# Kernel tuning notes

Hardware: AMD Instinct MI355X
Metric: run time of the kernel (lower is better)

Reference implementation:

```python
import jax, jax.numpy as jnp
import numpy as np

N, D, H, DEG = 20000, 128, 128, 32


def setup_inputs() -> dict:
    key = jax.random.key(0)
    ks = jax.random.split(key, 6)
    s = 0.02
    h = jax.random.normal(ks[0], (N, D), dtype=jnp.float32)
    # per-node neighbor indices, sorted by index (permutation invariance per docstring)
    nbr_idx = jnp.sort(jax.random.randint(ks[1], (N, DEG), 0, N), axis=-1)
    W_ih = jax.random.normal(ks[2], (4 * H, D), dtype=jnp.float32) * s
    W_hh = jax.random.normal(ks[3], (4 * H, H), dtype=jnp.float32) * s
    b_ih = jnp.zeros((4 * H,), jnp.float32)
    b_hh = jnp.zeros((4 * H,), jnp.float32)
    W_out = jax.random.normal(ks[4], (H, D + H), dtype=jnp.float32) * s
    b_out = jnp.zeros((H,), jnp.float32)
    return {"h": h, "nbr_idx": nbr_idx, "W_ih": W_ih, "W_hh": W_hh,
            "b_ih": b_ih, "b_hh": b_hh, "W_out": W_out, "b_out": b_out}


def reference(h, nbr_idx, W_ih, W_hh, b_ih, b_hh, W_out, b_out):
    # Gather neighbor features: [N, DEG, D]
    nbr = h[nbr_idx]
    # Precompute input-to-gate projections for all steps: [N, DEG, 4H]
    xg = jnp.einsum('ndi,gi->ndg', nbr, W_ih) + b_ih + b_hh
    xg = jnp.swapaxes(xg, 0, 1)  # [DEG, N, 4H] for scan over neighbor sequence
    h0 = jnp.zeros((h.shape[0], W_hh.shape[1]), h.dtype)
    c0 = jnp.zeros_like(h0)

    def step(carry, g_t):
        hp, cp = carry
        g = g_t + hp @ W_hh.T            # [N, 4H]
        i, f, gg, o = jnp.split(g, 4, axis=-1)  # PyTorch gate order i,f,g,o
        c = jax.nn.sigmoid(f) * cp + jax.nn.sigmoid(i) * jnp.tanh(gg)
        hn = jax.nn.sigmoid(o) * jnp.tanh(c)
        return (hn, c), None

    (agg, _), _ = jax.lax.scan(step, (h0, c0), xg)  # agg = final hidden state [N, H]
    combined = jnp.concatenate([h, agg], axis=-1)   # [N, D+H]
    return jax.nn.relu(combined @ W_out.T + b_out)  # [N, H]
```

## Files before the change

### kernel.cpp

```cpp
#include <hip/hip_runtime.h>

#define NN 20000
#define DD 128
#define HH 128
#define G4 512
#define DEG 32
#define NPB 32
#define PAIRS 625
#define GRID2 512
#define XTRA (PAIRS-GRID2)

typedef __attribute__((ext_vector_type(4))) float f32x4;
typedef __attribute__((ext_vector_type(8))) short s16x8;

#ifndef __has_builtin
#define __has_builtin(x) 0
#endif

static __device__ __forceinline__ float fexp2(float x){
#if __has_builtin(__builtin_amdgcn_exp2f)
  return __builtin_amdgcn_exp2f(x);
#else
  return exp2f(x);
#endif
}
static __device__ __forceinline__ float frcp(float x){
#if __has_builtin(__builtin_amdgcn_rcpf)
  return __builtin_amdgcn_rcpf(x);
#else
  return 1.f/x;
#endif
}

static __device__ __forceinline__ unsigned cvt_pk_bf16(float lo, float hi){
  unsigned r;
  asm("v_cvt_pk_bf16_f32 %0, %1, %2" : "=v"(r) : "v"(lo), "v"(hi));
  return r;
}
static __device__ __forceinline__ s16x8 ld8bf(const float* __restrict__ p){
  f32x4 a = *(const f32x4*)p;
  f32x4 b = *(const f32x4*)(p+4);
  union{unsigned u[4]; s16x8 v;} z;
  z.u[0]=cvt_pk_bf16(a[0],a[1]);
  z.u[1]=cvt_pk_bf16(a[2],a[3]);
  z.u[2]=cvt_pk_bf16(b[0],b[1]);
  z.u[3]=cvt_pk_bf16(b[2],b[3]);
  return z.v;
}
static __device__ __forceinline__ float lo16f(unsigned u){
  union{unsigned x; float f;} v; v.x = u << 16; return v.f;
}
static __device__ __forceinline__ float hi16f(unsigned u){
  union{unsigned x; float f;} v; v.x = u & 0xffff0000u; return v.f;
}
#define NLOG2E -1.44269504f
#define TLOG2E  2.88539008f

__global__ __launch_bounds__(512,2) void k_hp(
    const float* __restrict__ h, const float* __restrict__ W_ih,
    const float* __restrict__ b_ih, const float* __restrict__ b_hh,
    unsigned short* __restrict__ Hp)
{
  const int tid=threadIdx.x, w=tid>>6, lane=tid&63, lo=lane&15, hi=lane>>4;
  s16x8 A[4][4];
#pragma unroll
  for(int g=0;g<4;++g){
    const float* wr=W_ih+(size_t)(128*g+16*w+lo)*DD+8*hi;
#pragma unroll
    for(int c=0;c<4;++c) A[g][c]=ld8bf(wr+32*c);
  }
  f32x4 bb[4];
#pragma unroll
  for(int g=0;g<4;++g){
    const int gcb=128*g+16*w+4*hi;
    bb[g]=*(const f32x4*)(b_ih+gcb) + *(const f32x4*)(b_hh+gcb);
  }
  const int nchunk = (blockIdx.x < 57) ? 2 : 1;
  for(int cc=0; cc<nchunk; ++cc){
    const int n0 = ((cc? 256+blockIdx.x : blockIdx.x))*64;
    f32x4 acc[4][4];
#pragma unroll
    for(int g=0;g<4;++g)
#pragma unroll
      for(int nt=0;nt<4;++nt) acc[g][nt]=(f32x4)0.f;
#pragma unroll
    for(int c=0;c<4;++c){
      s16x8 B[4];
#pragma unroll
      for(int nt=0;nt<4;++nt){
        int nd=n0+16*nt+lo; if(nd>=NN) nd=NN-1;
        B[nt]=ld8bf(h+(size_t)nd*DD+32*c+8*hi);
      }
#pragma unroll
      for(int g=0;g<4;++g)
#pragma unroll
        for(int nt=0;nt<4;++nt)
          acc[g][nt]=__builtin_amdgcn_mfma_f32_16x16x32_bf16(A[g][c],B[nt],acc[g][nt],0,0,0);
    }
#pragma unroll
    for(int nt=0;nt<4;++nt){
      int nd=n0+16*nt+lo;
      if(nd<NN){
        unsigned short* p = Hp + (size_t)nd*G4 + w*64 + hi*16;
        uint4 q0, q1;
        q0.x=cvt_pk_bf16(acc[0][nt][0]+bb[0][0], acc[0][nt][1]+bb[0][1]);
        q0.y=cvt_pk_bf16(acc[0][nt][2]+bb[0][2], acc[0][nt][3]+bb[0][3]);
        q0.z=cvt_pk_bf16(acc[1][nt][0]+bb[1][0], acc[1][nt][1]+bb[1][1]);
        q0.w=cvt_pk_bf16(acc[1][nt][2]+bb[1][2], acc[1][nt][3]+bb[1][3]);
        q1.x=cvt_pk_bf16(acc[2][nt][0]+bb[2][0], acc[2][nt][1]+bb[2][1]);
        q1.y=cvt_pk_bf16(acc[2][nt][2]+bb[2][2], acc[2][nt][3]+bb[2][3]);
        q1.z=cvt_pk_bf16(acc[3][nt][0]+bb[3][0], acc[3][nt][1]+bb[3][1]);
        q1.w=cvt_pk_bf16(acc[3][nt][2]+bb[3][2], acc[3][nt][3]+bb[3][3]);
        *(uint4*)p = q0;
        *(uint4*)(p+8) = q1;
      }
    }
  }
}

static __device__ __forceinline__ void unpack_acc(const uint4 q[2], f32x4 acc[4]){
  acc[0][0]=lo16f(q[0].x); acc[0][1]=hi16f(q[0].x); acc[0][2]=lo16f(q[0].y); acc[0][3]=hi16f(q[0].y);
  acc[1][0]=lo16f(q[0].z); acc[1][1]=hi16f(q[0].z); acc[1][2]=lo16f(q[0].w); acc[1][3]=hi16f(q[0].w);
  acc[2][0]=lo16f(q[1].x); acc[2][1]=hi16f(q[1].x); acc[2][2]=lo16f(q[1].y); acc[2][3]=hi16f(q[1].y);
  acc[3][0]=lo16f(q[1].z); acc[3][1]=hi16f(q[1].z); acc[3][2]=lo16f(q[1].w); acc[3][3]=hi16f(q[1].w);
}

__global__ __launch_bounds__(512,2) void k_lstm(
    const float* __restrict__ h, const int* __restrict__ nbr,
    const float* __restrict__ W_hh, const unsigned short* __restrict__ Hp,
    const float* __restrict__ W_out, const float* __restrict__ b_out,
    float* __restrict__ out)
{
  __shared__ unsigned short hpA[16*HH];
  __shared__ unsigned short hpB[16*HH];
  __shared__ int nlds[DEG*NPB];
  const int tid=threadIdx.x, w=tid>>6, lane=tid&63, lo=lane&15, hi=lane>>4;
  const int swz=(lo&7)<<4;

  s16x8 A[4][4];
#pragma unroll
  for(int g=0;g<4;++g){
    const float* wr=W_hh+(size_t)(128*g+16*w+lo)*HH+8*hi;
#pragma unroll
    for(int c=0;c<4;++c) A[g][c]=ld8bf(wr+32*c);
  }

  const int npair = (blockIdx.x < XTRA) ? 2 : 1;
  for(int pp=0; pp<npair; ++pp){
    const int pidx = pp ? (GRID2 + blockIdx.x) : blockIdx.x;
    const int n0 = pidx*NPB;

    __syncthreads();
    {
      unsigned* za=(unsigned*)&hpA[0];
      unsigned* zb=(unsigned*)&hpB[0];
      za[tid]=0u; za[tid+512]=0u;
      zb[tid]=0u; zb[tid+512]=0u;
#pragma unroll
      for(int i=0;i<2;++i){
        int idx=tid+512*i;
        nlds[(idx&31)*NPB + (idx>>5)] = nbr[n0*DEG + idx];
      }
    }
    __syncthreads();

    float cstA[4]={0.f,0.f,0.f,0.f}, cstB[4]={0.f,0.f,0.f,0.f};
    f32x4 accB[4];
#pragma unroll
    for(int g=0;g<4;++g) accB[g]=(f32x4)0.f;

    uint4 qA0[2], qA1[2], qB0[2], qB1[2];
    {
      int ia0=nlds[lo],        ib0=nlds[16+lo];
      int ia1=nlds[NPB+lo],    ib1=nlds[NPB+16+lo];
      const unsigned short* g0=Hp+(size_t)ia0*G4+w*64+hi*16;
      const unsigned short* g1=Hp+(size_t)ib0*G4+w*64+hi*16;
      const unsigned short* g2=Hp+(size_t)ia1*G4+w*64+hi*16;
      const unsigned short* g3=Hp+(size_t)ib1*G4+w*64+hi*16;
      qA0[0]=*(const uint4*)g0; qA0[1]=*(const uint4*)(g0+8);
      qB0[0]=*(const uint4*)g1; qB0[1]=*(const uint4*)(g1+8);
      qA1[0]=*(const uint4*)g2; qA1[1]=*(const uint4*)(g2+8);
      qB1[0]=*(const uint4*)g3; qB1[1]=*(const uint4*)(g3+8);
    }

    for(int t=0;t<DEG;++t){
      const int tn2 = (t+2<DEG)? t+2 : DEG-1;
      int ia2=nlds[tn2*NPB + lo];
      int ib2=nlds[tn2*NPB + 16 + lo];
      uint4 qA2[2];
      {
        const unsigned short* gp=Hp+(size_t)ia2*G4+w*64+hi*16;
        qA2[0]=*(const uint4*)gp; qA2[1]=*(const uint4*)(gp+8);
      }
      s16x8 Ba[4];
      const char* ra=(const char*)&hpA[0];
#pragma unroll
      for(int c=0;c<4;++c)
        Ba[c]=*(const s16x8*)(ra + ((lo*256 + 64*c + 16*hi) ^ swz));
      {
        float hv[4];
#pragma unroll
        for(int r=0;r<4;++r){
          float ei=fexp2(accB[0][r]*NLOG2E);
          float ef=fexp2(accB[1][r]*NLOG2E);
          float eg=fexp2(accB[2][r]*TLOG2E);
          float eo=fexp2(accB[3][r]*NLOG2E);
          float itg=(eg-1.f)*frcp((1.f+ei)*(1.f+eg));
          float cc=cstB[r]*frcp(1.f+ef)+itg;
          cstB[r]=cc;
          float ec=fexp2(cc*TLOG2E);
          hv[r]=(ec-1.f)*frcp((1.f+eo)*(1.f+ec));
        }
        uint2 pk;
        pk.x=cvt_pk_bf16(hv[0],hv[1]);
        pk.y=cvt_pk_bf16(hv[2],hv[3]);
        char* wb=(char*)&hpB[0];
        *(uint2*)(wb + ((lo*256 + 32*w + 8*hi) ^ swz)) = pk;
      }
      f32x4 accA[4];
      unpack_acc(qA0, accA);
#pragma unroll
      for(int c=0;c<4;++c)
#pragma unroll
        for(int g=0;g<4;++g)
          accA[g]=__builtin_amdgcn_mfma_f32_16x16x32_bf16(A[g][c],Ba[c],accA[g],0,0,0);
      qA0[0]=qA1[0]; qA0[1]=qA1[1]; qA1[0]=qA2[0]; qA1[1]=qA2[1];
      asm volatile("s_waitcnt lgkmcnt(0)\n\ts_barrier" ::: "memory");

      uint4 qB2[2];
      {
        const unsigned short* gp=Hp+(size_t)ib2*G4+w*64+hi*16;
        qB2[0]=*(const uint4*)gp; qB2[1]=*(const uint4*)(gp+8);
      }
      s16x8 Bb[4];
      const char* rb=(const char*)&hpB[0];
#pragma unroll
      for(int c=0;c<4;++c)
        Bb[c]=*(const s16x8*)(rb + ((lo*256 + 64*c + 16*hi) ^ swz));
      {
        float hv[4];
#pragma unroll
        for(int r=0;r<4;++r){
          float ei=fexp2(accA[0][r]*NLOG2E);
          float ef=fexp2(accA[1][r]*NLOG2E);
          float eg=fexp2(accA[2][r]*TLOG2E);
          float eo=fexp2(accA[3][r]*NLOG2E);
          float itg=(eg-1.f)*frcp((1.f+ei)*(1.f+eg));
          float cc=cstA[r]*frcp(1.f+ef)+itg;
          cstA[r]=cc;
          float ec=fexp2(cc*TLOG2E);
          hv[r]=(ec-1.f)*frcp((1.f+eo)*(1.f+ec));
        }
        uint2 pk;
        pk.x=cvt_pk_bf16(hv[0],hv[1]);
        pk.y=cvt_pk_bf16(hv[2],hv[3]);
        char* wb=(char*)&hpA[0];
        *(uint2*)(wb + ((lo*256 + 32*w + 8*hi) ^ swz)) = pk;
      }
      unpack_acc(qB0, accB);
#pragma unroll
      for(int c=0;c<4;++c)
#pragma unroll
        for(int g=0;g<4;++g)
          accB[g]=__builtin_amdgcn_mfma_f32_16x16x32_bf16(A[g][c],Bb[c],accB[g],0,0,0);
      qB0[0]=qB1[0]; qB0[1]=qB1[1]; qB1[0]=qB2[0]; qB1[1]=qB2[1];
      asm volatile("s_waitcnt lgkmcnt(0)\n\ts_barrier" ::: "memory");
    }

    {
      float hv[4];
#pragma unroll
      for(int r=0;r<4;++r){
        float ei=fexp2(accB[0][r]*NLOG2E);
        float ef=fexp2(accB[1][r]*NLOG2E);
        float eg=fexp2(accB[2][r]*TLOG2E);
        float eo=fexp2(accB[3][r]*NLOG2E);
        float itg=(eg-1.f)*frcp((1.f+ei)*(1.f+eg));
        float cc=cstB[r]*frcp(1.f+ef)+itg;
        float ec=fexp2(cc*TLOG2E);
        hv[r]=(ec-1.f)*frcp((1.f+eo)*(1.f+ec));
      }
      uint2 pk;
      pk.x=cvt_pk_bf16(hv[0],hv[1]);
      pk.y=cvt_pk_bf16(hv[2],hv[3]);
      char* wb=(char*)&hpB[0];
      *(uint2*)(wb + ((lo*256 + 32*w + 8*hi) ^ swz)) = pk;
    }
    asm volatile("s_waitcnt lgkmcnt(0)\n\ts_barrier" ::: "memory");

    s16x8 AO[8];
    {
      const float* wr=W_out+(size_t)(16*w+lo)*256+8*hi;
#pragma unroll
      for(int c=0;c<8;++c) AO[c]=ld8bf(wr+32*c);
    }
    const int ob=16*w+4*hi;
    f32x4 bias=*(const f32x4*)(b_out+ob);
#pragma unroll
    for(int nt=0;nt<2;++nt){
      const int node=n0+nt*16+lo;
      s16x8 BB[8];
      const float* hr=h+(size_t)node*DD+8*hi;
#pragma unroll
      for(int c=0;c<4;++c) BB[c]=ld8bf(hr+32*c);
      const char* rb=(const char*)(nt? &hpB[0] : &hpA[0]);
#pragma unroll
      for(int c=0;c<4;++c)
        BB[4+c]=*(const s16x8*)(rb + ((lo*256 + 64*c + 16*hi) ^ swz));
      f32x4 acc=(f32x4)0.f;
#pragma unroll
      for(int c=0;c<8;++c) acc=__builtin_amdgcn_mfma_f32_16x16x32_bf16(AO[c],BB[c],acc,0,0,0);
#pragma unroll
      for(int r=0;r<4;++r){ float v=acc[r]+bias[r]; acc[r]=v>0.f?v:0.f; }
      *(f32x4*)(out+(size_t)node*HH+ob)=acc;
    }
  }
}

extern "C" void kernel_launch(void* const* d_in, const int* in_sizes, int n_in,
                              void* d_out, int out_size, void* d_ws, size_t ws_size,
                              hipStream_t stream)
{
  const float* h     = (const float*)d_in[0];
  const int*   nbr   = (const int*)d_in[1];
  const float* W_ih  = (const float*)d_in[2];
  const float* W_hh  = (const float*)d_in[3];
  const float* b_ih  = (const float*)d_in[4];
  const float* b_hh  = (const float*)d_in[5];
  const float* W_out = (const float*)d_in[6];
  const float* b_out = (const float*)d_in[7];
  unsigned short* Hp = (unsigned short*)d_ws;

  k_hp<<<256, 512, 0, stream>>>(h, W_ih, b_ih, b_hh, Hp);
  k_lstm<<<GRID2, 512, 0, stream>>>(h, nbr, W_hh, Hp, W_out, b_out, (float*)d_out);
}
```

Before: 227.8 us.

## Launch one block per pair with higher occupancy and shallower prefetch

Replaces the 512-block grid, where some blocks handled two node pairs, with one block per pair (625 blocks), and raises launch bounds from 2 to 6 blocks per CU. The gather prefetch depth drops from two steps to one to cut register use, and neighbor indices are pre-multiplied by the row stride when staged in LDS. The goal is to remove the tail imbalance from blocks doing double work and to hide gather and barrier latency through more resident waves. The cost is less latency hiding within each wave and possible spilling if the tighter register budget is too small.

Result: slower. 811.7 us (+256.2%).

```diff
diff --git a/kernel.cpp b/kernel.cpp
--- a/kernel.cpp
+++ b/kernel.cpp
@@ -7,8 +7,6 @@
 #define DEG 32
 #define NPB 32
 #define PAIRS 625
-#define GRID2 512
-#define XTRA (PAIRS-GRID2)
 
 typedef __attribute__((ext_vector_type(4))) float f32x4;
 typedef __attribute__((ext_vector_type(8))) short s16x8;
@@ -125,7 +123,7 @@
   acc[3][0]=lo16f(q[1].z); acc[3][1]=hi16f(q[1].z); acc[3][2]=lo16f(q[1].w); acc[3][3]=hi16f(q[1].w);
 }
 
-__global__ __launch_bounds__(512,2) void k_lstm(
+__global__ __launch_bounds__(512,6) void k_lstm(
     const float* __restrict__ h, const int* __restrict__ nbr,
     const float* __restrict__ W_hh, const unsigned short* __restrict__ Hp,
     const float* __restrict__ W_out, const float* __restrict__ b_out,
@@ -135,7 +133,9 @@
   __shared__ unsigned short hpB[16*HH];
   __shared__ int nlds[DEG*NPB];
   const int tid=threadIdx.x, w=tid>>6, lane=tid&63, lo=lane&15, hi=lane>>4;
+  const int n0=blockIdx.x*NPB;
   const int swz=(lo&7)<<4;
+  const int woff=w*64+hi*16;
 
   s16x8 A[4][4];
 #pragma unroll
@@ -144,129 +144,44 @@
 #pragma unroll
     for(int c=0;c<4;++c) A[g][c]=ld8bf(wr+32*c);
   }
-
-  const int npair = (blockIdx.x < XTRA) ? 2 : 1;
-  for(int pp=0; pp<npair; ++pp){
-    const int pidx = pp ? (GRID2 + blockIdx.x) : blockIdx.x;
-    const int n0 = pidx*NPB;
-
-    __syncthreads();
+  {
+    unsigned* za=(unsigned*)&hpA[0];
+    unsigned* zb=(unsigned*)&hpB[0];
+    za[tid]=0u; za[tid+512]=0u;
+    zb[tid]=0u; zb[tid+512]=0u;
+#pragma unroll
+    for(int i=0;i<2;++i){
+      int idx=tid+512*i;
+      nlds[(idx&31)*NPB + (idx>>5)] = nbr[n0*DEG + idx]*G4;
+    }
+  }
+  __syncthreads();
+
+  float cstA[4]={0.f,0.f,0.f,0.f}, cstB[4]={0.f,0.f,0.f,0.f};
+  f32x4 accB[4];
+#pragma unroll
+  for(int g=0;g<4;++g) accB[g]=(f32x4)0.f;
+
+  uint4 qA0[2], qB0[2];
+  {
+    const unsigned short* ga=Hp+(size_t)nlds[lo]+woff;
+    const unsigned short* gb=Hp+(size_t)nlds[16+lo]+woff;
+    qA0[0]=*(const uint4*)ga; qA0[1]=*(const uint4*)(ga+8);
+    qB0[0]=*(const uint4*)gb; qB0[1]=*(const uint4*)(gb+8);
+  }
+
+  for(int t=0;t<DEG;++t){
+    const int tn = (t+1<DEG)? t+1 : t;
+    uint4 qA1[2];
     {
-      unsigned* za=(unsigned*)&hpA[0];
-      unsigned* zb=(unsigned*)&hpB[0];
-      za[tid]=0u; za[tid+512]=0u;
-      zb[tid]=0u; zb[tid+512]=0u;
-#pragma unroll
-      for(int i=0;i<2;++i){
-        int idx=tid+512*i;
-        nlds[(idx&31)*NPB + (idx>>5)] = nbr[n0*DEG + idx];
-      }
-    }
-    __syncthreads();
-
-    float cstA[4]={0.f,0.f,0.f,0.f}, cstB[4]={0.f,0.f,0.f,0.f};
-    f32x4 accB[4];
-#pragma unroll
-    for(int g=0;g<4;++g) accB[g]=(f32x4)0.f;
-
-    uint4 qA0[2], qA1[2], qB0[2], qB1[2];
-    {
-      int ia0=nlds[lo],        ib0=nlds[16+lo];
-      int ia1=nlds[NPB+lo],    ib1=nlds[NPB+16+lo];
-      const unsigned short* g0=Hp+(size_t)ia0*G4+w*64+hi*16;
-      const unsigned short* g1=Hp+(size_t)ib0*G4+w*64+hi*16;
-      const unsigned short* g2=Hp+(size_t)ia1*G4+w*64+hi*16;
-      const unsigned short* g3=Hp+(size_t)ib1*G4+w*64+hi*16;
-      qA0[0]=*(const uint4*)g0; qA0[1]=*(const uint4*)(g0+8);
-      qB0[0]=*(const uint4*)g1; qB0[1]=*(const uint4*)(g1+8);
-      qA1[0]=*(const uint4*)g2; qA1[1]=*(const uint4*)(g2+8);
-      qB1[0]=*(const uint4*)g3; qB1[1]=*(const uint4*)(g3+8);
-    }
-
-    for(int t=0;t<DEG;++t){
-      const int tn2 = (t+2<DEG)? t+2 : DEG-1;
-      int ia2=nlds[tn2*NPB + lo];
-      int ib2=nlds[tn2*NPB + 16 + lo];
-      uint4 qA2[2];
-      {
-        const unsigned short* gp=Hp+(size_t)ia2*G4+w*64+hi*16;
-        qA2[0]=*(const uint4*)gp; qA2[1]=*(const uint4*)(gp+8);
-      }
-      s16x8 Ba[4];
-      const char* ra=(const char*)&hpA[0];
-#pragma unroll
-      for(int c=0;c<4;++c)
-        Ba[c]=*(const s16x8*)(ra + ((lo*256 + 64*c + 16*hi) ^ swz));
-      {
-        float hv[4];
-#pragma unroll
-        for(int r=0;r<4;++r){
-          float ei=fexp2(accB[0][r]*NLOG2E);
-          float ef=fexp2(accB[1][r]*NLOG2E);
-          float eg=fexp2(accB[2][r]*TLOG2E);
-          float eo=fexp2(accB[3][r]*NLOG2E);
-          float itg=(eg-1.f)*frcp((1.f+ei)*(1.f+eg));
-          float cc=cstB[r]*frcp(1.f+ef)+itg;
-          cstB[r]=cc;
-          float ec=fexp2(cc*TLOG2E);
-          hv[r]=(ec-1.f)*frcp((1.f+eo)*(1.f+ec));
-        }
-        uint2 pk;
-        pk.x=cvt_pk_bf16(hv[0],hv[1]);
-        pk.y=cvt_pk_bf16(hv[2],hv[3]);
-        char* wb=(char*)&hpB[0];
-        *(uint2*)(wb + ((lo*256 + 32*w + 8*hi) ^ swz)) = pk;
-      }
-      f32x4 accA[4];
-      unpack_acc(qA0, accA);
-#pragma unroll
-      for(int c=0;c<4;++c)
-#pragma unroll
-        for(int g=0;g<4;++g)
-          accA[g]=__builtin_amdgcn_mfma_f32_16x16x32_bf16(A[g][c],Ba[c],accA[g],0,0,0);
-      qA0[0]=qA1[0]; qA0[1]=qA1[1]; qA1[0]=qA2[0]; qA1[1]=qA2[1];
-      asm volatile("s_waitcnt lgkmcnt(0)\n\ts_barrier" ::: "memory");
-
-      uint4 qB2[2];
-      {
-        const unsigned short* gp=Hp+(size_t)ib2*G4+w*64+hi*16;
-        qB2[0]=*(const uint4*)gp; qB2[1]=*(const uint4*)(gp+8);
-      }
-      s16x8 Bb[4];
-      const char* rb=(const char*)&hpB[0];
-#pragma unroll
-      for(int c=0;c<4;++c)
-        Bb[c]=*(const s16x8*)(rb + ((lo*256 + 64*c + 16*hi) ^ swz));
-      {
-        float hv[4];
-#pragma unroll
-        for(int r=0;r<4;++r){
-          float ei=fexp2(accA[0][r]*NLOG2E);
-          float ef=fexp2(accA[1][r]*NLOG2E);
-          float eg=fexp2(accA[2][r]*TLOG2E);
-          float eo=fexp2(accA[3][r]*NLOG2E);
-          float itg=(eg-1.f)*frcp((1.f+ei)*(1.f+eg));
-          float cc=cstA[r]*frcp(1.f+ef)+itg;
-          cstA[r]=cc;
-          float ec=fexp2(cc*TLOG2E);
-          hv[r]=(ec-1.f)*frcp((1.f+eo)*(1.f+ec));
-        }
-        uint2 pk;
-        pk.x=cvt_pk_bf16(hv[0],hv[1]);
-        pk.y=cvt_pk_bf16(hv[2],hv[3]);
-        char* wb=(char*)&hpA[0];
-        *(uint2*)(wb + ((lo*256 + 32*w + 8*hi) ^ swz)) = pk;
-      }
-      unpack_acc(qB0, accB);
-#pragma unroll
-      for(int c=0;c<4;++c)
-#pragma unroll
-        for(int g=0;g<4;++g)
-          accB[g]=__builtin_amdgcn_mfma_f32_16x16x32_bf16(A[g][c],Bb[c],accB[g],0,0,0);
-      qB0[0]=qB1[0]; qB0[1]=qB1[1]; qB1[0]=qB2[0]; qB1[1]=qB2[1];
-      asm volatile("s_waitcnt lgkmcnt(0)\n\ts_barrier" ::: "memory");
-    }
-
+      const unsigned short* gp=Hp+(size_t)nlds[tn*NPB+lo]+woff;
+      qA1[0]=*(const uint4*)gp; qA1[1]=*(const uint4*)(gp+8);
+    }
+    s16x8 Ba[4];
+    const char* ra=(const char*)&hpA[0];
+#pragma unroll
+    for(int c=0;c<4;++c)
+      Ba[c]=*(const s16x8*)(ra + ((lo*256 + 64*c + 16*hi) ^ swz));
     {
       float hv[4];
 #pragma unroll
@@ -277,6 +192,7 @@
         float eo=fexp2(accB[3][r]*NLOG2E);
         float itg=(eg-1.f)*frcp((1.f+ei)*(1.f+eg));
         float cc=cstB[r]*frcp(1.f+ef)+itg;
+        cstB[r]=cc;
         float ec=fexp2(cc*TLOG2E);
         hv[r]=(ec-1.f)*frcp((1.f+eo)*(1.f+ec));
       }
@@ -286,34 +202,102 @@
       char* wb=(char*)&hpB[0];
       *(uint2*)(wb + ((lo*256 + 32*w + 8*hi) ^ swz)) = pk;
     }
+    f32x4 accA[4];
+    unpack_acc(qA0, accA);
+#pragma unroll
+    for(int c=0;c<4;++c)
+#pragma unroll
+      for(int g=0;g<4;++g)
+        accA[g]=__builtin_amdgcn_mfma_f32_16x16x32_bf16(A[g][c],Ba[c],accA[g],0,0,0);
+    qA0[0]=qA1[0]; qA0[1]=qA1[1];
     asm volatile("s_waitcnt lgkmcnt(0)\n\ts_barrier" ::: "memory");
 
-    s16x8 AO[8];
+    uint4 qB1[2];
     {
-      const float* wr=W_out+(size_t)(16*w+lo)*256+8*hi;
-#pragma unroll
-      for(int c=0;c<8;++c) AO[c]=ld8bf(wr+32*c);
-    }
-    const int ob=16*w+4*hi;
-    f32x4 bias=*(const f32x4*)(b_out+ob);
-#pragma unroll
-    for(int nt=0;nt<2;++nt){
-      const int node=n0+nt*16+lo;
-      s16x8 BB[8];
-      const float* hr=h+(size_t)node*DD+8*hi;
-#pragma unroll
-      for(int c=0;c<4;++c) BB[c]=ld8bf(hr+32*c);
-      const char* rb=(const char*)(nt? &hpB[0] : &hpA[0]);
-#pragma unroll
-      for(int c=0;c<4;++c)
-        BB[4+c]=*(const s16x8*)(rb + ((lo*256 + 64*c + 16*hi) ^ swz));
-      f32x4 acc=(f32x4)0.f;
-#pragma unroll
-      for(int c=0;c<8;++c) acc=__builtin_amdgcn_mfma_f32_16x16x32_bf16(AO[c],BB[c],acc,0,0,0);
-#pragma unroll
-      for(int r=0;r<4;++r){ float v=acc[r]+bias[r]; acc[r]=v>0.f?v:0.f; }
-      *(f32x4*)(out+(size_t)node*HH+ob)=acc;
-    }
+      const unsigned short* gp=Hp+(size_t)nlds[tn*NPB+16+lo]+woff;
+      qB1[0]=*(const uint4*)gp; qB1[1]=*(const uint4*)(gp+8);
+    }
+    s16x8 Bb[4];
+    const char* rb=(const char*)&hpB[0];
+#pragma unroll
+    for(int c=0;c<4;++c)
+      Bb[c]=*(const s16x8*)(rb + ((lo*256 + 64*c + 16*hi) ^ swz));
+    {
+      float hv[4];
+#pragma unroll
+      for(int r=0;r<4;++r){
+        float ei=fexp2(accA[0][r]*NLOG2E);
+        float ef=fexp2(accA[1][r]*NLOG2E);
+        float eg=fexp2(accA[2][r]*TLOG2E);
+        float eo=fexp2(accA[3][r]*NLOG2E);
+        float itg=(eg-1.f)*frcp((1.f+ei)*(1.f+eg));
+        float cc=cstA[r]*frcp(1.f+ef)+itg;
+        cstA[r]=cc;
+        float ec=fexp2(cc*TLOG2E);
+        hv[r]=(ec-1.f)*frcp((1.f+eo)*(1.f+ec));
+      }
+      uint2 pk;
+      pk.x=cvt_pk_bf16(hv[0],hv[1]);
+      pk.y=cvt_pk_bf16(hv[2],hv[3]);
+      char* wb=(char*)&hpA[0];
+      *(uint2*)(wb + ((lo*256 + 32*w + 8*hi) ^ swz)) = pk;
+    }
+    unpack_acc(qB0, accB);
+#pragma unroll
+    for(int c=0;c<4;++c)
+#pragma unroll
+      for(int g=0;g<4;++g)
+        accB[g]=__builtin_amdgcn_mfma_f32_16x16x32_bf16(A[g][c],Bb[c],accB[g],0,0,0);
+    qB0[0]=qB1[0]; qB0[1]=qB1[1];
+    asm volatile("s_waitcnt lgkmcnt(0)\n\ts_barrier" ::: "memory");
+  }
+
+  {
+    float hv[4];
+#pragma unroll
+    for(int r=0;r<4;++r){
+      float ei=fexp2(accB[0][r]*NLOG2E);
+      float ef=fexp2(accB[1][r]*NLOG2E);
+      float eg=fexp2(accB[2][r]*TLOG2E);
+      float eo=fexp2(accB[3][r]*NLOG2E);
+      float itg=(eg-1.f)*frcp((1.f+ei)*(1.f+eg));
+      float cc=cstB[r]*frcp(1.f+ef)+itg;
+      float ec=fexp2(cc*TLOG2E);
+      hv[r]=(ec-1.f)*frcp((1.f+eo)*(1.f+ec));
+    }
+    uint2 pk;
+    pk.x=cvt_pk_bf16(hv[0],hv[1]);
+    pk.y=cvt_pk_bf16(hv[2],hv[3]);
+    char* wb=(char*)&hpB[0];
+    *(uint2*)(wb + ((lo*256 + 32*w + 8*hi) ^ swz)) = pk;
+  }
+  asm volatile("s_waitcnt lgkmcnt(0)\n\ts_barrier" ::: "memory");
+
+  s16x8 AO[8];
+  {
+    const float* wr=W_out+(size_t)(16*w+lo)*256+8*hi;
+#pragma unroll
+    for(int c=0;c<8;++c) AO[c]=ld8bf(wr+32*c);
+  }
+  const int ob=16*w+4*hi;
+  f32x4 bias=*(const f32x4*)(b_out+ob);
+#pragma unroll
+  for(int nt=0;nt<2;++nt){
+    const int node=n0+nt*16+lo;
+    s16x8 BB[8];
+    const float* hr=h+(size_t)node*DD+8*hi;
+#pragma unroll
+    for(int c=0;c<4;++c) BB[c]=ld8bf(hr+32*c);
+    const char* rb=(const char*)(nt? &hpB[0] : &hpA[0]);
+#pragma unroll
+    for(int c=0;c<4;++c)
+      BB[4+c]=*(const s16x8*)(rb + ((lo*256 + 64*c + 16*hi) ^ swz));
+    f32x4 acc=(f32x4)0.f;
+#pragma unroll
+    for(int c=0;c<8;++c) acc=__builtin_amdgcn_mfma_f32_16x16x32_bf16(AO[c],BB[c],acc,0,0,0);
+#pragma unroll
+    for(int r=0;r<4;++r){ float v=acc[r]+bias[r]; acc[r]=v>0.f?v:0.f; }
+    *(f32x4*)(out+(size_t)node*HH+ob)=acc;
   }
 }
 
@@ -332,5 +316,5 @@
   unsigned short* Hp = (unsigned short*)d_ws;
 
   k_hp<<<256, 512, 0, stream>>>(h, W_ih, b_ih, b_hh, Hp);
-  k_lstm<<<GRID2, 512, 0, stream>>>(h, nbr, W_hh, Hp, W_out, b_out, (float*)d_out);
-}
+  k_lstm<<<PAIRS, 512, 0, stream>>>(h, nbr, W_hh, Hp, W_out, b_out, (float*)d_out);
+}
```
